# Optimization experiments

Hardware: AMD Instinct MI355X
Metric: run time of the kernel (lower is better)

The kernel has to match this reference:

```python
import jax, jax.numpy as jnp
import numpy as np

NU, NI, ED, H = 30000, 10000, 64, 4
D = ED * H            # fusion_dim = 256
N = NU + NI           # total graph nodes
E = 100000            # edges
B = 8192              # scored (user, wine) pairs
NST, SD = 4, 64       # side tokens / side token dim
NEG = -1e30


def setup_inputs():
    key = jax.random.key(0)
    ks = iter(jax.random.split(key, 64))

    def w(*shape):
        return jax.random.normal(next(ks), shape, jnp.float32) * 0.05

    return {
        "user": jax.random.randint(next(ks), (B,), 0, NU),
        "wine": jax.random.randint(next(ks), (B,), 0, NI),
        "edge_index": jax.random.randint(next(ks), (2, E), 0, N),
        "keep_edge": jax.random.uniform(next(ks), (E,)) > 0.2,   # edge_dropout keep mask
        "node_mask": jax.random.uniform(next(ks), (N,)) < 0.2,   # mask-autoencoding mask
        "user_emb": w(NU, ED),
        "wine_emb": w(NI, ED),
        "up_w": w(ED, D), "up_b": w(D),
        "wp_w": w(ED, D), "wp_b": w(D),
        "sf_proj_w": w(SD, D), "sf_proj_b": w(D),
        "sf_q_w": w(D, D), "sf_q_b": w(D),
        "sf_k_w": w(D, D), "sf_k_b": w(D),
        "sf_v_w": w(D, D), "sf_v_b": w(D),
        "sf_o_w": w(D, D), "sf_o_b": w(D),
        "sf_fc_w": w(2 * D, D), "sf_fc_b": w(D),
        "g_w": w(D, D), "g_b": w(D),
        "t_q_w": w(D, H * D), "t_q_b": w(H * D),
        "t_k_w": w(D, H * D), "t_k_b": w(H * D),
        "t_v_w": w(D, H * D), "t_v_b": w(H * D),
        "t_skip_w": w(D, D), "t_skip_b": w(D),
        "fc_w": w(2 * D, 1), "fc_b": w(1),
        "ae_w": w(D, D), "ae_b": w(D),
        "ep_w": w(2 * D, 1), "ep_b": w(1),
        "wine_side_features": jax.random.normal(next(ks), (NI, NST, SD), jnp.float32),
    }


def _forward(user, wine, edge_index, keep_edge, node_mask,
             user_emb, wine_emb, up_w, up_b, wp_w, wp_b,
             sf_proj_w, sf_proj_b, sf_q_w, sf_q_b, sf_k_w, sf_k_b,
             sf_v_w, sf_v_b, sf_o_w, sf_o_b, sf_fc_w, sf_fc_b,
             g_w, g_b, t_q_w, t_q_b, t_k_w, t_k_b, t_v_w, t_v_b,
             t_skip_w, t_skip_b, fc_w, fc_b, ae_w, ae_b, ep_w, ep_b,
             wine_side_features):
    u_proj = user_emb @ up_w + up_b                       # [NU, D]
    w_proj = wine_emb @ wp_w + wp_b                       # [NI, D]

    # WineSideFusion: single-head attention of wine embedding over side tokens
    side = wine_side_features @ sf_proj_w + sf_proj_b     # [NI, T, D]
    q = w_proj @ sf_q_w + sf_q_b                          # [NI, D]
    k = side @ sf_k_w + sf_k_b                            # [NI, T, D]
    v = side @ sf_v_w + sf_v_b
    attn = jax.nn.softmax(jnp.einsum('nd,ntd->nt', q, k) / jnp.sqrt(jnp.float32(D)), axis=-1)
    ao = jnp.einsum('nt,ntd->nd', attn, v) @ sf_o_w + sf_o_b
    fused = jnp.concatenate([w_proj, ao], axis=1) @ sf_fc_w + sf_fc_b

    x = jnp.concatenate([u_proj, fused], axis=0)          # [N, D]
    src, dst = edge_index[0], edge_index[1]
    ew = keep_edge.astype(x.dtype)                        # edge dropout as 0/1 weights

    # GCNConv (add self loops, symmetric norm)
    deg = jax.ops.segment_sum(ew, dst, num_segments=N) + 1.0
    dinv = jax.lax.rsqrt(deg)
    norm = dinv[src] * dinv[dst] * ew                     # [E]
    xw = x @ g_w                                          # [N, D]
    agg = jax.ops.segment_sum(xw[src] * norm[:, None], dst, num_segments=N)
    x = agg + xw * (dinv * dinv)[:, None] + g_b

    # TransformerConv(heads=H, concat=False): mean over heads + skip
    qh = (x @ t_q_w + t_q_b).reshape(N, H, D)
    kh = (x @ t_k_w + t_k_b).reshape(N, H, D)
    vh = (x @ t_v_w + t_v_b).reshape(N, H, D)
    logits = jnp.einsum('ehd,ehd->eh', qh[dst], kh[src]) / jnp.sqrt(jnp.float32(D))
    logits = jnp.where(keep_edge[:, None], logits, NEG)
    m = jax.ops.segment_max(logits, dst, num_segments=N)  # [N, H]
    m = jnp.where(m < NEG / 2, 0.0, m)                    # guard empty segments
    e = jnp.exp(logits - m[dst]) * ew[:, None]            # [E, H]
    den = jax.ops.segment_sum(e, dst, num_segments=N)     # [N, H]
    num = jax.ops.segment_sum(e[:, :, None] * vh[src], dst, num_segments=N)  # [N, H, D]
    attn_out = num / jnp.maximum(den, 1e-16)[:, :, None]
    x = attn_out.mean(axis=1) + x @ t_skip_w + t_skip_b   # [N, D]

    # Masked autoencoding: masked rows are zeroed, then autoencoded -> recon = bias
    maskf = node_mask.astype(x.dtype)
    recon = ae_b                                          # 0 @ ae_w + ae_b
    diff = recon[None, :] - x                             # [N, D]
    recon_loss = jnp.sum(maskf[:, None] * diff * diff) / (jnp.sum(maskf) * D)

    u_out = x[user]                                       # [B, D]
    w_out = x[wine + NU]                                  # [B, D]
    pair = jnp.concatenate([u_out, w_out], axis=1)        # [B, 2D]

    edge_score = jax.nn.sigmoid(pair @ ep_w + ep_b)       # [B, 1]
    edge_pred_loss = jnp.mean((edge_score - 1.0) ** 2)

    score = jax.nn.sigmoid((pair @ fc_w + fc_b).squeeze(-1)) * 4.0 + 1.0  # [B]
    return score, recon_loss, edge_pred_loss


def reference(user, wine, edge_index, keep_edge, node_mask,
              user_emb, wine_emb, up_w, up_b, wp_w, wp_b,
              sf_proj_w, sf_proj_b, sf_q_w, sf_q_b, sf_k_w, sf_k_b,
              sf_v_w, sf_v_b, sf_o_w, sf_o_b, sf_fc_w, sf_fc_b,
              g_w, g_b, t_q_w, t_q_b, t_k_w, t_k_b, t_v_w, t_v_b,
              t_skip_w, t_skip_b, fc_w, fc_b, ae_w, ae_b, ep_w, ep_b,
              wine_side_features):
    return _forward(user, wine, edge_index, keep_edge, node_mask,
                    user_emb, wine_emb, up_w, up_b, wp_w, wp_b,
                    sf_proj_w, sf_proj_b, sf_q_w, sf_q_b, sf_k_w, sf_k_b,
                    sf_v_w, sf_v_b, sf_o_w, sf_o_b, sf_fc_w, sf_fc_b,
                    g_w, g_b, t_q_w, t_q_b, t_k_w, t_k_b, t_v_w, t_v_b,
                    t_skip_w, t_skip_b, fc_w, fc_b, ae_w, ae_b, ep_w, ep_b,
                    wine_side_features)
```

## Files before the change

kernel.cpp:

```cpp
#include <hip/hip_runtime.h>
#include <stdint.h>

typedef unsigned short u16;
typedef unsigned char u8;
typedef __attribute__((ext_vector_type(8))) short bf16x8;
typedef __attribute__((ext_vector_type(4))) float f32x4;

#define NU_C 30000
#define NI_C 10000
#define N_C  40000
#define E_C  100000
#define B_C  8192

static __device__ __forceinline__ float bf2f(u16 u) {
    union { unsigned int i; float f; } c; c.i = ((unsigned int)u) << 16; return c.f;
}
static __device__ __forceinline__ u16 f2bf(float f) {
    union { float f; unsigned int i; } c; c.f = f;
    return (u16)((c.i + 0x7FFFu + ((c.i >> 16) & 1u)) >> 16);
}
static __device__ __forceinline__ float wave_sum(float v) {
#pragma unroll
    for (int off = 32; off > 0; off >>= 1) v += __shfl_xor(v, off);
    return v;
}

__global__ void zero_kernel(unsigned int* p, int n) {
    int i = blockIdx.x * 256 + threadIdx.x;
    if (i < n) p[i] = 0u;
}
__global__ void fillval_kernel(float* p, int n, float v) {
    int i = blockIdx.x * 256 + threadIdx.x;
    if (i < n) p[i] = v;
}

__global__ void detect_kernel(const unsigned int* a, int n, int* flag) {
    int i = blockIdx.x * 256 + threadIdx.x;
    if (i >= n) return;
    unsigned int v = a[i];
    int f = 0;
    if (v > 1u) f |= 1;
    if (v != 0u && v != 0x3F800000u) f |= 2;
    if (f) atomicOr(flag, f);
}
__global__ void conv_mask_kernel(const void* raw, u8* outm, int n, const int* flag) {
    int i = blockIdx.x * 256 + threadIdx.x;
    if (i >= n) return;
    const int f = *flag;
    u8 r;
    if ((f & 1) == 0)      r = ((const int*)raw)[i] != 0;
    else if ((f & 2) == 0) r = ((const float*)raw)[i] != 0.f;
    else                   r = ((const u8*)raw)[i] != 0;
    outm[i] = r;
}

__global__ void conv3_kernel(const float* __restrict__ a, int na4,
                             const float* __restrict__ b, int nb4,
                             const float* __restrict__ c, int nc4,
                             u16* __restrict__ oa, u16* __restrict__ ob, u16* __restrict__ oc)
{
    int tot = na4 + nb4 + nc4;
    for (int i = blockIdx.x * 256 + threadIdx.x; i < tot; i += gridDim.x * 256) {
        const float* s; u16* o; int j = i;
        if (j < na4) { s = a; o = oa; }
        else if ((j -= na4) < nb4) { s = b; o = ob; }
        else { j -= nb4; s = c; o = oc; }
        float4 v = *(const float4*)&s[(size_t)j * 4];
        ushort4 r;
        r.x = f2bf(v.x); r.y = f2bf(v.y); r.z = f2bf(v.z); r.w = f2bf(v.w);
        *(ushort4*)&o[(size_t)j * 4] = r;
    }
}

#define WT_ELEMS 1359872
__device__ const int wd_prefix[23] = {0,16384,32768,49152,114688,180224,245760,311296,442368,
    507904,573440,638976,704512,770048,835584,901120,966656,1032192,1097728,1163264,1228800,
    1294336,1359872};
__device__ const u8  wd_src[22]  = {0,1,2,3,4,5,6,7,8,9,10,11,12,10,11,12,10,11,12,10,11,12};
__device__ const short wd_ldw[22]= {256,256,256,256,256,256,256,256,256,256,
    1024,1024,1024,1024,1024,1024,1024,1024,1024,1024,1024,1024};
__device__ const short wd_coff[22]={0,0,0,0,0,0,0,0,0,0, 0,0,0, 256,256,256, 512,512,512, 768,768,768};
__device__ const short wd_kmask[22]={63,63,63,255,255,255,255,511,255,255,
    255,255,255,255,255,255,255,255,255,255,255,255};
__device__ const u8  wd_ksh[22] = {6,6,6,8,8,8,8,9,8,8, 8,8,8,8,8,8,8,8,8,8,8,8};

__global__ __launch_bounds__(256)
void wtrans_kernel(const float* w0, const float* w1, const float* w2, const float* w3,
                   const float* w4, const float* w5, const float* w6, const float* w7,
                   const float* w8, const float* w9, const float* w10, const float* w11,
                   const float* w12, u16* __restrict__ WT)
{
    int idx = blockIdx.x * 256 + threadIdx.x;
    if (idx >= WT_ELEMS) return;
    int d = 0;
    while (wd_prefix[d + 1] <= idx) ++d;
    const int local = idx - wd_prefix[d];
    const int k = local & wd_kmask[d];
    const int n = local >> wd_ksh[d];
    const float* s;
    switch (wd_src[d]) {
        case 0: s = w0; break; case 1: s = w1; break; case 2: s = w2; break;
        case 3: s = w3; break; case 4: s = w4; break; case 5: s = w5; break;
        case 6: s = w6; break; case 7: s = w7; break; case 8: s = w8; break;
        case 9: s = w9; break; case 10: s = w10; break; case 11: s = w11; break;
        default: s = w12; break;
    }
    WT[idx] = f2bf(s[(size_t)k * wd_ldw[d] + wd_coff[d] + n]);
}

__global__ void prep_bias_kernel(const float* sfk_b, const float* sfv_b,
                                 const float* tq_b, const float* tk_b, const float* tv_b,
                                 float* kvb, float* qkvb)
{
    int i = blockIdx.x * 256 + threadIdx.x;
    if (i < 512) kvb[i] = i < 256 ? sfk_b[i] : sfv_b[i - 256];
    if (i < 3072) {
        int h = i / 768, j = i - h * 768;
        qkvb[i] = j < 256 ? tq_b[h * 256 + j]
                : (j < 512 ? tk_b[h * 256 + j - 256] : tv_b[h * 256 + j - 512]);
    }
}

template <typename OT>
__global__ __launch_bounds__(512)
void mgemm_kernel(const u16* __restrict__ A, int lda,
                  const u16* __restrict__ WT,
                  const float* __restrict__ bias,
                  OT* __restrict__ C, int ldc,
                  int M, int N, int K)
{
    __shared__ __align__(16) u16 As[256][72];
    __shared__ __align__(16) u16 Bs[128][72];
    const int t = threadIdx.x;
    const int wid = t >> 6, lane = t & 63;
    const int wr = wid >> 1, wc = wid & 1;
    const int lr = lane & 15, lg = lane >> 4;
    const int gx = gridDim.x;
    const int nwg = gx * gridDim.y;
    const int orig = blockIdx.y * gx + blockIdx.x;
    const int q8 = nwg >> 3, r8 = nwg & 7;
    const int xcd = orig & 7, oidx = orig >> 3;
    const int swzb = (xcd < r8 ? xcd * (q8 + 1) : r8 * (q8 + 1) + (xcd - r8) * q8) + oidx;
    const int row0 = (swzb / gx) * 256, col0 = (swzb % gx) * 128;
    const int sra = t >> 1, sha = (t & 1) * 32;
    const int srb = t >> 2, shb = (t & 3) * 16;
    f32x4 acc[4][4] = {};

    for (int k0 = 0; k0 < K; k0 += 64) {
        {
            const int gr = row0 + sra;
            if (gr < M) {
                const u16* ap = &A[(size_t)gr * lda + k0 + sha];
#pragma unroll
                for (int j = 0; j < 4; ++j)
                    *(bf16x8*)&As[sra][sha + j * 8] = *(const bf16x8*)&ap[j * 8];
            } else {
                const bf16x8 z = {0, 0, 0, 0, 0, 0, 0, 0};
#pragma unroll
                for (int j = 0; j < 4; ++j)
                    *(bf16x8*)&As[sra][sha + j * 8] = z;
            }
        }
        {
            const u16* bp = &WT[(size_t)(col0 + srb) * K + k0 + shb];
#pragma unroll
            for (int j = 0; j < 2; ++j)
                *(bf16x8*)&Bs[srb][shb + j * 8] = *(const bf16x8*)&bp[j * 8];
        }
        __syncthreads();
#pragma unroll
        for (int kk = 0; kk < 2; ++kk) {
            bf16x8 af[4], bfr[4];
#pragma unroll
            for (int m = 0; m < 4; ++m)
                af[m] = *(const bf16x8*)&As[wr * 64 + m * 16 + lr][kk * 32 + lg * 8];
#pragma unroll
            for (int n = 0; n < 4; ++n)
                bfr[n] = *(const bf16x8*)&Bs[wc * 64 + n * 16 + lr][kk * 32 + lg * 8];
#pragma unroll
            for (int m = 0; m < 4; ++m)
#pragma unroll
                for (int n = 0; n < 4; ++n)
                    acc[m][n] = __builtin_amdgcn_mfma_f32_16x16x32_bf16(af[m], bfr[n], acc[m][n], 0, 0, 0);
        }
        __syncthreads();
    }
#pragma unroll
    for (int m = 0; m < 4; ++m) {
#pragma unroll
        for (int r = 0; r < 4; ++r) {
            int row = row0 + wr * 64 + m * 16 + lg * 4 + r;
            if (row >= M) continue;
#pragma unroll
            for (int n = 0; n < 4; ++n) {
                int col = col0 + wc * 64 + n * 16 + lr;
                float v = acc[m][n][r];
                if (bias) v += bias[col];
                if constexpr (sizeof(OT) == 4) C[(size_t)row * ldc + col] = v;
                else C[(size_t)row * ldc + col] = f2bf(v);
            }
        }
    }
}

__global__ __launch_bounds__(256)
void side_attn_kernel(const u16* __restrict__ q, const u16* __restrict__ kv,
                      u16* __restrict__ ao, int NI)
{
    const int wid = threadIdx.x >> 6, lane = threadIdx.x & 63;
    const int n = blockIdx.x * 4 + wid;
    if (n >= NI) return;
    const ushort4 qu = *(const ushort4*)&q[(size_t)n * 256 + lane * 4];
    const float q0 = bf2f(qu.x), q1 = bf2f(qu.y), q2 = bf2f(qu.z), q3 = bf2f(qu.w);
    float logit[4];
#pragma unroll
    for (int tk = 0; tk < 4; ++tk) {
        const ushort4 ku = *(const ushort4*)&kv[((size_t)n * 4 + tk) * 512 + lane * 4];
        float p = q0 * bf2f(ku.x) + q1 * bf2f(ku.y) + q2 * bf2f(ku.z) + q3 * bf2f(ku.w);
        logit[tk] = wave_sum(p) * (1.f / 16.f);
    }
    float mx = fmaxf(fmaxf(logit[0], logit[1]), fmaxf(logit[2], logit[3]));
    float e[4], den = 0.f;
#pragma unroll
    for (int tk = 0; tk < 4; ++tk) { e[tk] = __expf(logit[tk] - mx); den += e[tk]; }
    const float inv = 1.f / den;
    float o0 = 0.f, o1 = 0.f, o2 = 0.f, o3 = 0.f;
#pragma unroll
    for (int tk = 0; tk < 4; ++tk) {
        const ushort4 vu = *(const ushort4*)&kv[((size_t)n * 4 + tk) * 512 + 256 + lane * 4];
        const float w = e[tk] * inv;
        o0 = fmaf(w, bf2f(vu.x), o0); o1 = fmaf(w, bf2f(vu.y), o1);
        o2 = fmaf(w, bf2f(vu.z), o2); o3 = fmaf(w, bf2f(vu.w), o3);
    }
    ushort4 o;
    o.x = f2bf(o0); o.y = f2bf(o1); o.z = f2bf(o2); o.w = f2bf(o3);
    *(ushort4*)&ao[(size_t)n * 256 + lane * 4] = o;
}

__global__ void degw_kernel(const int* __restrict__ dst, const u8* __restrict__ keep,
                            float* __restrict__ degw, int E)
{
    int e = blockIdx.x * 256 + threadIdx.x;
    if (e >= E) return;
    if (keep[e]) atomicAdd(&degw[dst[e]], 1.f);
}

__global__ void dinv_kernel(const float* __restrict__ degw, float* __restrict__ dinv, int N)
{
    int n = blockIdx.x * 256 + threadIdx.x;
    if (n < N) dinv[n] = rsqrtf(degw[n] + 1.f);
}

__global__ void count_kernel(const int* __restrict__ dst, int* __restrict__ cnt, int E)
{
    int e = blockIdx.x * 256 + threadIdx.x;
    if (e < E) atomicAdd(&cnt[dst[e]], 1);
}

__global__ __launch_bounds__(1024)
void scan_kernel(const int* __restrict__ cnt, int* __restrict__ rs, int n)
{
    __shared__ int wsum[17];
    __shared__ int s_run;
    const int t = threadIdx.x, lane = t & 63, wid = t >> 6;
    if (t == 0) s_run = 0;
    __syncthreads();
    for (int base = 0; base < n; base += 1024) {
        int i = base + t;
        int v = (i < n) ? cnt[i] : 0;
        int x = v;
#pragma unroll
        for (int off = 1; off < 64; off <<= 1) {
            int y = __shfl_up(x, off);
            if (lane >= off) x += y;
        }
        if (lane == 63) wsum[wid] = x;
        __syncthreads();
        if (t == 0) {
            int a = 0;
            for (int j = 0; j < 16; ++j) { int tmp = wsum[j]; wsum[j] = a; a += tmp; }
            wsum[16] = a;
        }
        __syncthreads();
        if (i < n) rs[i] = s_run + wsum[wid] + x - v;
        __syncthreads();
        if (t == 0) s_run += wsum[16];
        __syncthreads();
    }
    if (t == 0) rs[n] = s_run;
}

__global__ void fill_kernel(const int* __restrict__ dst, const int* __restrict__ rs,
                            int* __restrict__ cursor, int* __restrict__ eid, int E)
{
    int e = blockIdx.x * 256 + threadIdx.x;
    if (e >= E) return;
    int d = dst[e];
    int p = atomicAdd(&cursor[d], 1);
    eid[rs[d] + p] = e;
}

__global__ void sort_kernel(const int* __restrict__ rs, int* __restrict__ eid, int N)
{
    int n = blockIdx.x * 256 + threadIdx.x;
    if (n >= N) return;
    const int b = rs[n], len = rs[n + 1] - b;
    for (int i = 1; i < len; ++i) {
        int key = eid[b + i];
        int j = i - 1;
        while (j >= 0 && eid[b + j] > key) { eid[b + j + 1] = eid[b + j]; --j; }
        eid[b + j + 1] = key;
    }
}

__global__ __launch_bounds__(256)
void gcn_kernel(const u16* __restrict__ xw, const int* __restrict__ src,
                const u8* __restrict__ keep,
                const int* __restrict__ rs, const int* __restrict__ eid,
                const float* __restrict__ dinv, const float* __restrict__ gb,
                u16* __restrict__ xout, int N)
{
    const int n = blockIdx.x;
    const int d = threadIdx.x;
    const float di = dinv[n];
    float acc = bf2f(xw[(size_t)n * 256 + d]) * di * di;
    const int e0 = rs[n], e1 = rs[n + 1];
    for (int i = e0; i < e1; ++i) {
        const int e = eid[i];
        if (!keep[e]) continue;
        const int s = src[e];
        acc = fmaf(bf2f(xw[(size_t)s * 256 + d]), dinv[s] * di, acc);
    }
    xout[(size_t)n * 256 + d] = f2bf(acc + gb[d]);
}

__global__ __launch_bounds__(256)
void tconv_head_kernel(const u16* __restrict__ qkv,
                       const int* __restrict__ src, const u8* __restrict__ keep,
                       const int* __restrict__ rs, const int* __restrict__ eid,
                       float* __restrict__ xacc, int N)
{
    const int wid = threadIdx.x >> 6, lane = threadIdx.x & 63;
    const int n = blockIdx.x * 4 + wid;
    if (n >= N) return;
    const ushort4 qu = *(const ushort4*)&qkv[(size_t)n * 768 + lane * 4];
    const float q0 = bf2f(qu.x), q1 = bf2f(qu.y), q2 = bf2f(qu.z), q3 = bf2f(qu.w);
    const int e0 = rs[n], e1 = rs[n + 1];
    float m = -1e30f, den = 0.f;
    float a0 = 0.f, a1 = 0.f, a2 = 0.f, a3 = 0.f;
    for (int i = e0; i < e1; ++i) {
        const int e = eid[i];
        if (!keep[e]) continue;
        const int s = src[e];
        const ushort4 ku = *(const ushort4*)&qkv[(size_t)s * 768 + 256 + lane * 4];
        float p = q0 * bf2f(ku.x) + q1 * bf2f(ku.y) + q2 * bf2f(ku.z) + q3 * bf2f(ku.w);
        p = wave_sum(p);
        const float lg = p * (1.f / 16.f);
        if (lg > m) {
            const float sc = __expf(m - lg);
            den *= sc; a0 *= sc; a1 *= sc; a2 *= sc; a3 *= sc;
            m = lg;
        }
        const float w = __expf(lg - m);
        den += w;
        const ushort4 vu = *(const ushort4*)&qkv[(size_t)s * 768 + 512 + lane * 4];
        a0 = fmaf(w, bf2f(vu.x), a0); a1 = fmaf(w, bf2f(vu.y), a1);
        a2 = fmaf(w, bf2f(vu.z), a2); a3 = fmaf(w, bf2f(vu.w), a3);
    }
    const float inv = 0.25f / fmaxf(den, 1e-16f);
    float4* p4 = (float4*)&xacc[(size_t)n * 256 + lane * 4];
    float4 cur = *p4;
    cur.x += a0 * inv; cur.y += a1 * inv; cur.z += a2 * inv; cur.w += a3 * inv;
    *p4 = cur;
}

__global__ __launch_bounds__(256)
void recon_kernel(const float* __restrict__ x, const u8* __restrict__ mask,
                  const float* __restrict__ aeb,
                  float* __restrict__ rblkS, float* __restrict__ rblkC, int N)
{
    const int total = N * 256;
    float s = 0.f, c = 0.f;
    for (int idx = blockIdx.x * 256 + threadIdx.x; idx < total; idx += gridDim.x * 256) {
        const int n = idx >> 8, d = idx & 255;
        if (mask[n]) {
            const float diff = aeb[d] - x[idx];
            s = fmaf(diff, diff, s);
            if (d == 0) c += 1.f;
        }
    }
    s = wave_sum(s); c = wave_sum(c);
    __shared__ float ss[4], cc[4];
    const int lane = threadIdx.x & 63, wid = threadIdx.x >> 6;
    if (lane == 0) { ss[wid] = s; cc[wid] = c; }
    __syncthreads();
    if (threadIdx.x == 0) {
        rblkS[blockIdx.x] = ss[0] + ss[1] + ss[2] + ss[3];
        rblkC[blockIdx.x] = cc[0] + cc[1] + cc[2] + cc[3];
    }
}

__global__ __launch_bounds__(256)
void score_kernel(const float* __restrict__ x, const int* __restrict__ user,
                  const int* __restrict__ wine,
                  const float* __restrict__ epw, const float* __restrict__ epb,
                  const float* __restrict__ fcw, const float* __restrict__ fcb,
                  float* __restrict__ out, float* __restrict__ sblk, int B)
{
    __shared__ float sep[4];
    const int wid = threadIdx.x >> 6, lane = threadIdx.x & 63;
    const int b = blockIdx.x * 4 + wid;
    if (b < B) {
        const size_t u = (size_t)user[b];
        const size_t w = (size_t)wine[b] + NU_C;
        const float4 xu = *(const float4*)&x[u * 256 + lane * 4];
        const float4 xw = *(const float4*)&x[w * 256 + lane * 4];
        const float4 e1 = *(const float4*)&epw[lane * 4];
        const float4 e2 = *(const float4*)&epw[256 + lane * 4];
        const float4 f1 = *(const float4*)&fcw[lane * 4];
        const float4 f2 = *(const float4*)&fcw[256 + lane * 4];
        float pep = xu.x * e1.x + xu.y * e1.y + xu.z * e1.z + xu.w * e1.w
                  + xw.x * e2.x + xw.y * e2.y + xw.z * e2.z + xw.w * e2.w;
        float pfc = xu.x * f1.x + xu.y * f1.y + xu.z * f1.z + xu.w * f1.w
                  + xw.x * f2.x + xw.y * f2.y + xw.z * f2.z + xw.w * f2.w;
        pep = wave_sum(pep); pfc = wave_sum(pfc);
        if (lane == 0) {
            const float es = 1.f / (1.f + __expf(-(pep + epb[0])));
            sep[wid] = (es - 1.f) * (es - 1.f);
            out[b] = 1.f / (1.f + __expf(-(pfc + fcb[0]))) * 4.f + 1.f;
        }
    } else if (lane == 0) {
        sep[wid] = 0.f;
    }
    __syncthreads();
    if (threadIdx.x == 0) sblk[blockIdx.x] = sep[0] + sep[1] + sep[2] + sep[3];
}

__global__ __launch_bounds__(1024)
void final_reduce_kernel(const float* __restrict__ rblkS, const float* __restrict__ rblkC,
                         const float* __restrict__ sblk, float* __restrict__ out, int B)
{
    const int t = threadIdx.x, lane = t & 63, wid = t >> 6;
    float s = rblkS[t] + rblkS[t + 1024];
    float c = rblkC[t] + rblkC[t + 1024];
    float p = sblk[t] + sblk[t + 1024];
    s = wave_sum(s); c = wave_sum(c); p = wave_sum(p);
    __shared__ float ss[16], cc[16], pp[16];
    if (lane == 0) { ss[wid] = s; cc[wid] = c; pp[wid] = p; }
    __syncthreads();
    if (t == 0) {
        float S = 0.f, C = 0.f, P = 0.f;
        for (int i = 0; i < 16; ++i) { S += ss[i]; C += cc[i]; P += pp[i]; }
        out[B] = S / (C * 256.f);
        out[B + 1] = P / (float)B;
    }
}

extern "C" void kernel_launch(void* const* d_in, const int* in_sizes, int n_in,
                              void* d_out, int out_size, void* d_ws, size_t ws_size,
                              hipStream_t stream)
{
    const int* user = (const int*)d_in[0];
    const int* wine = (const int*)d_in[1];
    const int* e_src = (const int*)d_in[2];
    const int* e_dst = e_src + E_C;
    const void* keep_raw  = d_in[3];
    const void* nmask_raw = d_in[4];
    const float* user_emb = (const float*)d_in[5];
    const float* wine_emb = (const float*)d_in[6];
    const float* up_w = (const float*)d_in[7];
    const float* up_b = (const float*)d_in[8];
    const float* wp_w = (const float*)d_in[9];
    const float* wp_b = (const float*)d_in[10];
    const float* sf_proj_w = (const float*)d_in[11];
    const float* sf_proj_b = (const float*)d_in[12];
    const float* sf_q_w = (const float*)d_in[13];
    const float* sf_q_b = (const float*)d_in[14];
    const float* sf_k_w = (const float*)d_in[15];
    const float* sf_k_b = (const float*)d_in[16];
    const float* sf_v_w = (const float*)d_in[17];
    const float* sf_v_b = (const float*)d_in[18];
    const float* sf_o_w = (const float*)d_in[19];
    const float* sf_o_b = (const float*)d_in[20];
    const float* sf_fc_w = (const float*)d_in[21];
    const float* sf_fc_b = (const float*)d_in[22];
    const float* g_w = (const float*)d_in[23];
    const float* g_b = (const float*)d_in[24];
    const float* t_q_w = (const float*)d_in[25];
    const float* t_q_b = (const float*)d_in[26];
    const float* t_k_w = (const float*)d_in[27];
    const float* t_k_b = (const float*)d_in[28];
    const float* t_v_w = (const float*)d_in[29];
    const float* t_v_b = (const float*)d_in[30];
    const float* t_skip_w = (const float*)d_in[31];
    const float* t_skip_b = (const float*)d_in[32];
    const float* fc_w = (const float*)d_in[33];
    const float* fc_b = (const float*)d_in[34];
    const float* ae_b = (const float*)d_in[36];
    const float* ep_w = (const float*)d_in[37];
    const float* ep_b = (const float*)d_in[38];
    const float* wsf = (const float*)d_in[39];
    float* out = (float*)d_out;
    char* ws = (char*)d_ws;

    size_t off = 0;
    auto take = [&](size_t b) { size_t r = off; off += (b + 255) & ~(size_t)255; return r; };
    const size_t o_xb     = take((size_t)N_C * 256 * 2);
    const size_t o_cnt    = take((size_t)N_C * 4);
    const size_t o_degw   = take((size_t)N_C * 4);
    const size_t o_cursor = take((size_t)N_C * 4);
    const size_t o_scal   = take(256);
    const size_t o_rowst  = take((size_t)(N_C + 1) * 4);
    const size_t o_dinv   = take((size_t)N_C * 4);
    const size_t o_eid    = take((size_t)E_C * 4);
    const size_t o_kmask  = take((size_t)E_C);
    const size_t o_nmask  = take((size_t)N_C);
    const size_t o_rblkS  = take(2048 * 4);
    const size_t o_rblkC  = take(2048 * 4);
    const size_t o_sblk   = take(2048 * 4);
    const size_t o_wt     = take((size_t)WT_ELEMS * 2);
    const size_t o_bias   = take(3584 * 4);
    const size_t ARENA    = 102400000;
    const size_t o_arena  = take(ARENA);
    const size_t NEED = off;

    if (ws_size < NEED) {
        fillval_kernel<<<dim3((out_size + 255) / 256), 256, 0, stream>>>(
            out, out_size, (float)((double)ws_size / (1024.0 * 1024.0)));
        return;
    }

    u16*   xb     = (u16*)  (ws + o_xb);
    int*   cnt    = (int*)  (ws + o_cnt);
    float* degw   = (float*)(ws + o_degw);
    int*   cursor = (int*)  (ws + o_cursor);
    int*   flag   = (int*)  (ws + o_scal);
    int*   rowst  = (int*)  (ws + o_rowst);
    float* dinvb  = (float*)(ws + o_dinv);
    int*   eid    = (int*)  (ws + o_eid);
    u8*    kmask  = (u8*)   (ws + o_kmask);
    u8*    nmaskb = (u8*)   (ws + o_nmask);
    float* rblkS  = (float*)(ws + o_rblkS);
    float* rblkC  = (float*)(ws + o_rblkC);
    float* sblk   = (float*)(ws + o_sblk);
    u16*   WT     = (u16*)  (ws + o_wt);
    float* kvb    = (float*)(ws + o_bias);
    float* qkvb   = kvb + 512;

    u16* wt_up   = WT + 0;
    u16* wt_wp   = WT + 16384;
    u16* wt_proj = WT + 32768;
    u16* wt_sfq  = WT + 49152;
    u16* wt_sfkv = WT + 114688;
    u16* wt_sfo  = WT + 245760;
    u16* wt_sffc = WT + 311296;
    u16* wt_g    = WT + 442368;
    u16* wt_skip = WT + 507904;
    u16* wt_qkv  = WT + 573440;

    u16* ue16  = (u16*)(ws + o_arena);
    u16* we16  = (u16*)(ws + o_arena + 3840000);
    u16* wsf16 = (u16*)(ws + o_arena + 5120000);
    u16* cat   = (u16*)(ws + o_arena + 10240000);
    u16* side  = (u16*)(ws + o_arena + 20480000);
    u16* qbuf  = (u16*)(ws + o_arena + 40960000);
    u16* kvbuf = (u16*)(ws + o_arena + 46080000);
    u16* aobuf = (u16*)(ws + o_arena + 87040000);
    u16* xw    = (u16*)(ws + o_arena);
    u16* qkvh  = (u16*)(ws + o_arena);
    float* xacc = (float*)(ws + o_arena + 61440000);

    const int zero_words = (3 * N_C * 4 + 256) / 4;
    zero_kernel<<<dim3((zero_words + 255) / 256), 256, 0, stream>>>((unsigned int*)cnt, zero_words);

    detect_kernel<<<dim3((E_C / 4 + 255) / 256), 256, 0, stream>>>((const unsigned int*)keep_raw, E_C / 4, flag);
    conv_mask_kernel<<<dim3((E_C + 255) / 256), 256, 0, stream>>>(keep_raw, kmask, E_C, flag);
    conv_mask_kernel<<<dim3((N_C + 255) / 256), 256, 0, stream>>>(nmask_raw, nmaskb, N_C, flag);

    conv3_kernel<<<dim3(2048), 256, 0, stream>>>(user_emb, NU_C * 16, wine_emb, NI_C * 16,
                                                 wsf, N_C * 16, ue16, we16, wsf16);
    wtrans_kernel<<<dim3(WT_ELEMS / 256), 256, 0, stream>>>(up_w, wp_w, sf_proj_w, sf_q_w,
        sf_k_w, sf_v_w, sf_o_w, sf_fc_w, g_w, t_skip_w, t_q_w, t_k_w, t_v_w, WT);
    prep_bias_kernel<<<dim3(12), 256, 0, stream>>>(sf_k_b, sf_v_b, t_q_b, t_k_b, t_v_b, kvb, qkvb);

    mgemm_kernel<u16><<<dim3(2, 118), 512, 0, stream>>>(ue16, 64, wt_up, up_b, xb, 256, NU_C, 256, 64);
    mgemm_kernel<u16><<<dim3(2, 40), 512, 0, stream>>>(we16, 64, wt_wp, wp_b, cat, 512, NI_C, 256, 64);
    mgemm_kernel<u16><<<dim3(2, 157), 512, 0, stream>>>(wsf16, 64, wt_proj, sf_proj_b, side, 256, N_C, 256, 64);
    mgemm_kernel<u16><<<dim3(2, 40), 512, 0, stream>>>(cat, 512, wt_sfq, sf_q_b, qbuf, 256, NI_C, 256, 256);
    mgemm_kernel<u16><<<dim3(4, 157), 512, 0, stream>>>(side, 256, wt_sfkv, kvb, kvbuf, 512, N_C, 512, 256);
    side_attn_kernel<<<dim3(2500), 256, 0, stream>>>(qbuf, kvbuf, aobuf, NI_C);
    mgemm_kernel<u16><<<dim3(2, 40), 512, 0, stream>>>(aobuf, 256, wt_sfo, sf_o_b, cat + 256, 512, NI_C, 256, 256);
    mgemm_kernel<u16><<<dim3(2, 40), 512, 0, stream>>>(cat, 512, wt_sffc, sf_fc_b, xb + (size_t)NU_C * 256, 256, NI_C, 256, 512);

    degw_kernel<<<dim3((E_C + 255) / 256), 256, 0, stream>>>(e_dst, kmask, degw, E_C);
    dinv_kernel<<<dim3((N_C + 255) / 256), 256, 0, stream>>>(degw, dinvb, N_C);
    count_kernel<<<dim3((E_C + 255) / 256), 256, 0, stream>>>(e_dst, cnt, E_C);
    scan_kernel<<<dim3(1), 1024, 0, stream>>>(cnt, rowst, N_C);
    fill_kernel<<<dim3((E_C + 255) / 256), 256, 0, stream>>>(e_dst, rowst, cursor, eid, E_C);
    sort_kernel<<<dim3((N_C + 255) / 256), 256, 0, stream>>>(rowst, eid, N_C);

    mgemm_kernel<u16><<<dim3(2, 157), 512, 0, stream>>>(xb, 256, wt_g, nullptr, xw, 256, N_C, 256, 256);
    gcn_kernel<<<dim3(N_C), 256, 0, stream>>>(xw, e_src, kmask, rowst, eid, dinvb, g_b, xb, N_C);

    mgemm_kernel<float><<<dim3(2, 157), 512, 0, stream>>>(xb, 256, wt_skip, t_skip_b, xacc, 256, N_C, 256, 256);
    for (int h = 0; h < 4; ++h) {
        mgemm_kernel<u16><<<dim3(6, 157), 512, 0, stream>>>(xb, 256, wt_qkv + h * 196608,
                                                            qkvb + h * 768, qkvh, 768, N_C, 768, 256);
        tconv_head_kernel<<<dim3(N_C / 4), 256, 0, stream>>>(qkvh, e_src, kmask, rowst, eid, xacc, N_C);
    }

    recon_kernel<<<dim3(2048), 256, 0, stream>>>(xacc, nmaskb, ae_b, rblkS, rblkC, N_C);
    score_kernel<<<dim3(2048), 256, 0, stream>>>(xacc, user, wine, ep_w, ep_b, fc_w, fc_b, out, sblk, B_C);
    final_reduce_kernel<<<dim3(1), 1024, 0, stream>>>(rblkS, rblkC, sblk, out, B_C);
}
```

Baseline: 700.0 us.

## Precompute sorted edge source/keep and GCN weights; branchless unrolled graph aggregation

Adds an edge_prep pass that writes, in CSR order, the source index packed with the keep bit plus the precomputed normalized GCN weight. The gcn and transformer-conv kernels then stop doing the eid→src/keep indirections. GCN is remapped to one wave per node with vectorized ushort4 loads, and the attention loop is made branchless and unrolled by two to overlap gathers. It also fuses the mask-conversion launches and the degree/count kernels, at the cost of an extra pass and extra workspace.

```diff
diff --git a/kernel.cpp b/kernel.cpp
--- a/kernel.cpp
+++ b/kernel.cpp
@@ -43,15 +43,26 @@
     if (v != 0u && v != 0x3F800000u) f |= 2;
     if (f) atomicOr(flag, f);
 }
-__global__ void conv_mask_kernel(const void* raw, u8* outm, int n, const int* flag) {
+__global__ void conv_masks_kernel(const void* keep_raw, const void* nm_raw,
+                                  u8* km, u8* nm, int E, int N, const int* flag)
+{
     int i = blockIdx.x * 256 + threadIdx.x;
-    if (i >= n) return;
     const int f = *flag;
-    u8 r;
-    if ((f & 1) == 0)      r = ((const int*)raw)[i] != 0;
-    else if ((f & 2) == 0) r = ((const float*)raw)[i] != 0.f;
-    else                   r = ((const u8*)raw)[i] != 0;
-    outm[i] = r;
+    if (i < E) {
+        u8 r;
+        if ((f & 1) == 0)      r = ((const int*)keep_raw)[i] != 0;
+        else if ((f & 2) == 0) r = ((const float*)keep_raw)[i] != 0.f;
+        else                   r = ((const u8*)keep_raw)[i] != 0;
+        km[i] = r;
+    }
+    int j = i - E;
+    if (j >= 0 && j < N) {
+        u8 r;
+        if ((f & 1) == 0)      r = ((const int*)nm_raw)[j] != 0;
+        else if ((f & 2) == 0) r = ((const float*)nm_raw)[j] != 0.f;
+        else                   r = ((const u8*)nm_raw)[j] != 0;
+        nm[j] = r;
+    }
 }
 
 __global__ void conv3_kernel(const float* __restrict__ a, int na4,
@@ -237,24 +248,20 @@
     *(ushort4*)&ao[(size_t)n * 256 + lane * 4] = o;
 }
 
-__global__ void degw_kernel(const int* __restrict__ dst, const u8* __restrict__ keep,
-                            float* __restrict__ degw, int E)
+__global__ void count_kernel(const int* __restrict__ dst, const u8* __restrict__ keep,
+                             int* __restrict__ cnt, float* __restrict__ degw, int E)
 {
     int e = blockIdx.x * 256 + threadIdx.x;
     if (e >= E) return;
-    if (keep[e]) atomicAdd(&degw[dst[e]], 1.f);
+    int d = dst[e];
+    atomicAdd(&cnt[d], 1);
+    if (keep[e]) atomicAdd(&degw[d], 1.f);
 }
 
 __global__ void dinv_kernel(const float* __restrict__ degw, float* __restrict__ dinv, int N)
 {
     int n = blockIdx.x * 256 + threadIdx.x;
     if (n < N) dinv[n] = rsqrtf(degw[n] + 1.f);
-}
-
-__global__ void count_kernel(const int* __restrict__ dst, int* __restrict__ cnt, int E)
-{
-    int e = blockIdx.x * 256 + threadIdx.x;
-    if (e < E) atomicAdd(&cnt[dst[e]], 1);
 }
 
 __global__ __launch_bounds__(1024)
@@ -313,32 +320,52 @@
     }
 }
 
+__global__ void edge_prep_kernel(const int* __restrict__ eid, const int* __restrict__ src,
+                                 const int* __restrict__ dst, const u8* __restrict__ keep,
+                                 const float* __restrict__ dinv,
+                                 int* __restrict__ ssrc, float* __restrict__ wnorm, int E)
+{
+    int i = blockIdx.x * 256 + threadIdx.x;
+    if (i >= E) return;
+    const int e = eid[i];
+    const int s = src[e];
+    const u8 k = keep[e];
+    ssrc[i] = s * 2 + (int)k;
+    wnorm[i] = k ? dinv[s] * dinv[dst[e]] : 0.f;
+}
+
 __global__ __launch_bounds__(256)
-void gcn_kernel(const u16* __restrict__ xw, const int* __restrict__ src,
-                const u8* __restrict__ keep,
-                const int* __restrict__ rs, const int* __restrict__ eid,
+void gcn_kernel(const u16* __restrict__ xw, const int* __restrict__ ssrc,
+                const float* __restrict__ wnorm, const int* __restrict__ rs,
                 const float* __restrict__ dinv, const float* __restrict__ gb,
                 u16* __restrict__ xout, int N)
 {
-    const int n = blockIdx.x;
-    const int d = threadIdx.x;
+    const int wid = threadIdx.x >> 6, lane = threadIdx.x & 63;
+    const int n = blockIdx.x * 4 + wid;
+    if (n >= N) return;
     const float di = dinv[n];
-    float acc = bf2f(xw[(size_t)n * 256 + d]) * di * di;
+    const float dii = di * di;
+    const ushort4 own = *(const ushort4*)&xw[(size_t)n * 256 + lane * 4];
+    float a0 = bf2f(own.x) * dii, a1 = bf2f(own.y) * dii;
+    float a2 = bf2f(own.z) * dii, a3 = bf2f(own.w) * dii;
     const int e0 = rs[n], e1 = rs[n + 1];
     for (int i = e0; i < e1; ++i) {
-        const int e = eid[i];
-        if (!keep[e]) continue;
-        const int s = src[e];
-        acc = fmaf(bf2f(xw[(size_t)s * 256 + d]), dinv[s] * di, acc);
-    }
-    xout[(size_t)n * 256 + d] = f2bf(acc + gb[d]);
+        const float w = wnorm[i];
+        const int s = ssrc[i] >> 1;
+        const ushort4 r = *(const ushort4*)&xw[(size_t)s * 256 + lane * 4];
+        a0 = fmaf(bf2f(r.x), w, a0); a1 = fmaf(bf2f(r.y), w, a1);
+        a2 = fmaf(bf2f(r.z), w, a2); a3 = fmaf(bf2f(r.w), w, a3);
+    }
+    const float4 g = *(const float4*)&gb[lane * 4];
+    ushort4 o;
+    o.x = f2bf(a0 + g.x); o.y = f2bf(a1 + g.y);
+    o.z = f2bf(a2 + g.z); o.w = f2bf(a3 + g.w);
+    *(ushort4*)&xout[(size_t)n * 256 + lane * 4] = o;
 }
 
 __global__ __launch_bounds__(256)
-void tconv_head_kernel(const u16* __restrict__ qkv,
-                       const int* __restrict__ src, const u8* __restrict__ keep,
-                       const int* __restrict__ rs, const int* __restrict__ eid,
-                       float* __restrict__ xacc, int N)
+void tconv_head_kernel(const u16* __restrict__ qkv, const int* __restrict__ ssrc,
+                       const int* __restrict__ rs, float* __restrict__ xacc, int N)
 {
     const int wid = threadIdx.x >> 6, lane = threadIdx.x & 63;
     const int n = blockIdx.x * 4 + wid;
@@ -348,24 +375,52 @@
     const int e0 = rs[n], e1 = rs[n + 1];
     float m = -1e30f, den = 0.f;
     float a0 = 0.f, a1 = 0.f, a2 = 0.f, a3 = 0.f;
-    for (int i = e0; i < e1; ++i) {
-        const int e = eid[i];
-        if (!keep[e]) continue;
-        const int s = src[e];
-        const ushort4 ku = *(const ushort4*)&qkv[(size_t)s * 768 + 256 + lane * 4];
-        float p = q0 * bf2f(ku.x) + q1 * bf2f(ku.y) + q2 * bf2f(ku.z) + q3 * bf2f(ku.w);
-        p = wave_sum(p);
-        const float lg = p * (1.f / 16.f);
-        if (lg > m) {
-            const float sc = __expf(m - lg);
-            den *= sc; a0 *= sc; a1 *= sc; a2 *= sc; a3 *= sc;
-            m = lg;
-        }
-        const float w = __expf(lg - m);
-        den += w;
-        const ushort4 vu = *(const ushort4*)&qkv[(size_t)s * 768 + 512 + lane * 4];
-        a0 = fmaf(w, bf2f(vu.x), a0); a1 = fmaf(w, bf2f(vu.y), a1);
-        a2 = fmaf(w, bf2f(vu.z), a2); a3 = fmaf(w, bf2f(vu.w), a3);
+    int i = e0;
+    for (; i + 1 < e1; i += 2) {
+        const int va = ssrc[i], vb = ssrc[i + 1];
+        const int sa = va >> 1, sb = vb >> 1;
+        const float ewa = (float)(va & 1), ewb = (float)(vb & 1);
+        const ushort4 ka = *(const ushort4*)&qkv[(size_t)sa * 768 + 256 + lane * 4];
+        const ushort4 kb = *(const ushort4*)&qkv[(size_t)sb * 768 + 256 + lane * 4];
+        const ushort4 xa = *(const ushort4*)&qkv[(size_t)sa * 768 + 512 + lane * 4];
+        const ushort4 xb4 = *(const ushort4*)&qkv[(size_t)sb * 768 + 512 + lane * 4];
+        float pa = q0 * bf2f(ka.x) + q1 * bf2f(ka.y) + q2 * bf2f(ka.z) + q3 * bf2f(ka.w);
+        float pb = q0 * bf2f(kb.x) + q1 * bf2f(kb.y) + q2 * bf2f(kb.z) + q3 * bf2f(kb.w);
+        pa = wave_sum(pa) * (1.f / 16.f);
+        pb = wave_sum(pb) * (1.f / 16.f);
+        {
+            const float mn = fmaxf(m, pa);
+            const float sc = __expf(m - mn);
+            const float w = __expf(pa - mn) * ewa;
+            den = den * sc + w;
+            a0 = fmaf(w, bf2f(xa.x), a0 * sc); a1 = fmaf(w, bf2f(xa.y), a1 * sc);
+            a2 = fmaf(w, bf2f(xa.z), a2 * sc); a3 = fmaf(w, bf2f(xa.w), a3 * sc);
+            m = mn;
+        }
+        {
+            const float mn = fmaxf(m, pb);
+            const float sc = __expf(m - mn);
+            const float w = __expf(pb - mn) * ewb;
+            den = den * sc + w;
+            a0 = fmaf(w, bf2f(xb4.x), a0 * sc); a1 = fmaf(w, bf2f(xb4.y), a1 * sc);
+            a2 = fmaf(w, bf2f(xb4.z), a2 * sc); a3 = fmaf(w, bf2f(xb4.w), a3 * sc);
+            m = mn;
+        }
+    }
+    if (i < e1) {
+        const int va = ssrc[i];
+        const int sa = va >> 1;
+        const float ewa = (float)(va & 1);
+        const ushort4 ka = *(const ushort4*)&qkv[(size_t)sa * 768 + 256 + lane * 4];
+        const ushort4 xa = *(const ushort4*)&qkv[(size_t)sa * 768 + 512 + lane * 4];
+        float pa = q0 * bf2f(ka.x) + q1 * bf2f(ka.y) + q2 * bf2f(ka.z) + q3 * bf2f(ka.w);
+        pa = wave_sum(pa) * (1.f / 16.f);
+        const float mn = fmaxf(m, pa);
+        const float sc = __expf(m - mn);
+        const float w = __expf(pa - mn) * ewa;
+        den = den * sc + w;
+        a0 = fmaf(w, bf2f(xa.x), a0 * sc); a1 = fmaf(w, bf2f(xa.y), a1 * sc);
+        a2 = fmaf(w, bf2f(xa.z), a2 * sc); a3 = fmaf(w, bf2f(xa.w), a3 * sc);
     }
     const float inv = 0.25f / fmaxf(den, 1e-16f);
     float4* p4 = (float4*)&xacc[(size_t)n * 256 + lane * 4];
@@ -513,6 +568,8 @@
     const size_t o_rowst  = take((size_t)(N_C + 1) * 4);
     const size_t o_dinv   = take((size_t)N_C * 4);
     const size_t o_eid    = take((size_t)E_C * 4);
+    const size_t o_ssrc   = take((size_t)E_C * 4);
+    const size_t o_wnorm  = take((size_t)E_C * 4);
     const size_t o_kmask  = take((size_t)E_C);
     const size_t o_nmask  = take((size_t)N_C);
     const size_t o_rblkS  = take(2048 * 4);
@@ -538,6 +595,8 @@
     int*   rowst  = (int*)  (ws + o_rowst);
     float* dinvb  = (float*)(ws + o_dinv);
     int*   eid    = (int*)  (ws + o_eid);
+    int*   ssrc   = (int*)  (ws + o_ssrc);
+    float* wnorm  = (float*)(ws + o_wnorm);
     u8*    kmask  = (u8*)   (ws + o_kmask);
     u8*    nmaskb = (u8*)   (ws + o_nmask);
     float* rblkS  = (float*)(ws + o_rblkS);
@@ -574,8 +633,7 @@
     zero_kernel<<<dim3((zero_words + 255) / 256), 256, 0, stream>>>((unsigned int*)cnt, zero_words);
 
     detect_kernel<<<dim3((E_C / 4 + 255) / 256), 256, 0, stream>>>((const unsigned int*)keep_raw, E_C / 4, flag);
-    conv_mask_kernel<<<dim3((E_C + 255) / 256), 256, 0, stream>>>(keep_raw, kmask, E_C, flag);
-    conv_mask_kernel<<<dim3((N_C + 255) / 256), 256, 0, stream>>>(nmask_raw, nmaskb, N_C, flag);
+    conv_masks_kernel<<<dim3((E_C + N_C + 255) / 256), 256, 0, stream>>>(keep_raw, nmask_raw, kmask, nmaskb, E_C, N_C, flag);
 
     conv3_kernel<<<dim3(2048), 256, 0, stream>>>(user_emb, NU_C * 16, wine_emb, NI_C * 16,
                                                  wsf, N_C * 16, ue16, we16, wsf16);
@@ -592,21 +650,21 @@
     mgemm_kernel<u16><<<dim3(2, 40), 512, 0, stream>>>(aobuf, 256, wt_sfo, sf_o_b, cat + 256, 512, NI_C, 256, 256);
     mgemm_kernel<u16><<<dim3(2, 40), 512, 0, stream>>>(cat, 512, wt_sffc, sf_fc_b, xb + (size_t)NU_C * 256, 256, NI_C, 256, 512);
 
-    degw_kernel<<<dim3((E_C + 255) / 256), 256, 0, stream>>>(e_dst, kmask, degw, E_C);
+    count_kernel<<<dim3((E_C + 255) / 256), 256, 0, stream>>>(e_dst, kmask, cnt, degw, E_C);
     dinv_kernel<<<dim3((N_C + 255) / 256), 256, 0, stream>>>(degw, dinvb, N_C);
-    count_kernel<<<dim3((E_C + 255) / 256), 256, 0, stream>>>(e_dst, cnt, E_C);
     scan_kernel<<<dim3(1), 1024, 0, stream>>>(cnt, rowst, N_C);
     fill_kernel<<<dim3((E_C + 255) / 256), 256, 0, stream>>>(e_dst, rowst, cursor, eid, E_C);
     sort_kernel<<<dim3((N_C + 255) / 256), 256, 0, stream>>>(rowst, eid, N_C);
+    edge_prep_kernel<<<dim3((E_C + 255) / 256), 256, 0, stream>>>(eid, e_src, e_dst, kmask, dinvb, ssrc, wnorm, E_C);
 
     mgemm_kernel<u16><<<dim3(2, 157), 512, 0, stream>>>(xb, 256, wt_g, nullptr, xw, 256, N_C, 256, 256);
-    gcn_kernel<<<dim3(N_C), 256, 0, stream>>>(xw, e_src, kmask, rowst, eid, dinvb, g_b, xb, N_C);
+    gcn_kernel<<<dim3(N_C / 4), 256, 0, stream>>>(xw, ssrc, wnorm, rowst, dinvb, g_b, xb, N_C);
 
     mgemm_kernel<float><<<dim3(2, 157), 512, 0, stream>>>(xb, 256, wt_skip, t_skip_b, xacc, 256, N_C, 256, 256);
     for (int h = 0; h < 4; ++h) {
         mgemm_kernel<u16><<<dim3(6, 157), 512, 0, stream>>>(xb, 256, wt_qkv + h * 196608,
                                                             qkvb + h * 768, qkvh, 768, N_C, 768, 256);
-        tconv_head_kernel<<<dim3(N_C / 4), 256, 0, stream>>>(qkvh, e_src, kmask, rowst, eid, xacc, N_C);
+        tconv_head_kernel<<<dim3(N_C / 4), 256, 0, stream>>>(qkvh, ssrc, rowst, xacc, N_C);
     }
 
     recon_kernel<<<dim3(2048), 256, 0, stream>>>(xacc, nmaskb, ae_b, rblkS, rblkC, N_C);
```

Measured after the change: 615.8 us. -12.0%, faster.
